# Optimization experiments

Measured on AMD Instinct MI355X. Metric: run time of the kernel, lower is better.

The kernel has to match this reference:

```python
import jax, jax.numpy as jnp
import numpy as np

NUM_QUBITS = 12
ENC_COPIES = 1
ANSATZ_COPIES = 2
BATCH = 1024
NUM_THETAS = NUM_QUBITS * (ANSATZ_COPIES + 1) * 2  # 72

_H = jnp.asarray(np.array([[1.0, 1.0], [1.0, -1.0]], np.complex64) / np.sqrt(2.0))


def _apply_1q(state, U, q):
    # state: [B, 2, 2, ..., 2] (n qubit axes); apply 2x2 unitary U on qubit q
    s = jnp.moveaxis(state, 1 + q, -1)
    s = jnp.einsum('...j,ij->...i', s, U)
    return jnp.moveaxis(s, -1, 1 + q)


def _apply_zpow(state, t, q):
    # cirq Z**t = diag(1, e^{i*pi*t}); t is scalar or per-batch [B]
    n = state.ndim - 1
    phase = jnp.exp(1j * jnp.pi * t).astype(jnp.complex64)
    factor = jnp.stack([jnp.ones_like(phase), phase], axis=-1)
    if factor.ndim == 2:  # batched exponent -> broadcast over other qubit axes
        factor = factor.reshape((factor.shape[0],) + (1,) * (n - 1) + (2,))
    s = jnp.moveaxis(state, 1 + q, -1)
    return jnp.moveaxis(s * factor, -1, 1 + q)


def _ypow_unitary(t):
    # cirq Y**t up to global phase e^{i*pi*t/2} (irrelevant for Z expectations)
    a = 0.5 * jnp.pi * t
    c, s = jnp.cos(a), jnp.sin(a)
    return jnp.stack([jnp.stack([c, -s]), jnp.stack([s, c])]).astype(jnp.complex64)


def _apply_cnot(state, c, t):
    s = jnp.moveaxis(state, (1 + c, 1 + t), (-2, -1))
    s = jnp.stack([s[..., 0, :], s[..., 1, ::-1]], axis=-2)
    return jnp.moveaxis(s, (-2, -1), (1 + c, 1 + t))


def _encoding_block(state, x):
    # FirstOrderPauliZEncoding: per copy, per qubit: H then Z**x_q
    for _ in range(ENC_COPIES):
        for q in range(NUM_QUBITS):
            state = _apply_1q(state, _H, q)
            state = _apply_zpow(state, x[:, q], q)
    return state


def _ansatz_block(state, th, with_cnot):
    # EfficientSU2 layer: Y**th[q,0], Z**th[q,1] per qubit, then CNOT chain
    for q in range(NUM_QUBITS):
        state = _apply_1q(state, _ypow_unitary(th[q, 0]), q)
        state = _apply_zpow(state, th[q, 1], q)
    if with_cnot:
        for q in range(NUM_QUBITS - 1):
            state = _apply_cnot(state, q, q + 1)
    return state


_enc = jax.checkpoint(_encoding_block)
_ans_cnot = jax.checkpoint(lambda st, th: _ansatz_block(st, th, True))
_ans_last = jax.checkpoint(lambda st, th: _ansatz_block(st, th, False))


def _circuit(inputs, thetas):
    b = inputs.shape[0]
    state = jnp.zeros((b, 2 ** NUM_QUBITS), jnp.complex64).at[:, 0].set(1.0)
    state = state.reshape((b,) + (2,) * NUM_QUBITS)
    state = _enc(state, inputs)
    th = thetas.reshape(ANSATZ_COPIES + 1, NUM_QUBITS, 2)
    for l in range(ANSATZ_COPIES + 1):
        state = (_ans_cnot if l < ANSATZ_COPIES else _ans_last)(state, th[l])
    # readouts: <Z_q> for each qubit
    probs = state.real ** 2 + state.imag ** 2
    exps = []
    for q in range(NUM_QUBITS):
        axes = tuple(a for a in range(1, NUM_QUBITS + 1) if a != 1 + q)
        p = probs.sum(axis=axes)  # [B, 2]
        exps.append(p[:, 0] - p[:, 1])
    return jnp.stack(exps, axis=-1)  # [B, NUM_QUBITS]


def setup_inputs() -> dict:
    key = jax.random.key(0)
    k1, k2 = jax.random.split(key)
    inputs = jax.random.uniform(k1, (BATCH, NUM_QUBITS), jnp.float32)
    thetas = jax.random.uniform(k2, (NUM_THETAS,), jnp.float32, minval=-1.0, maxval=1.0)
    return {"inputs": inputs, "thetas": thetas}


def reference(inputs, thetas):
    return _circuit(inputs, thetas)
```

## Files before the change

kernel.cpp:

```cpp
#include <hip/hip_runtime.h>


#define PI_F 3.14159265358979323846f
#define NR 32
#define PAD 66

__device__ __forceinline__ float2 cmul(float2 a, float2 b) {
    return make_float2(a.x*b.x - a.y*b.y, a.x*b.y + a.y*b.x);
}
__device__ __forceinline__ float2 cmulc(float2 a, float2 b) {
    return make_float2(a.x*b.x + a.y*b.y, a.y*b.x - a.x*b.y);
}

template<int RB>
__device__ __forceinline__ void ypow_reg(float2 (&a)[NR], float c, float s) {
    #pragma unroll
    for (int r0 = 0; r0 < NR; ++r0) {
        if ((r0 >> RB) & 1) continue;
        const int r1 = r0 | (1 << RB);
        float2 a0 = a[r0], a1 = a[r1];
        a[r0] = make_float2(c*a0.x - s*a1.x, c*a0.y - s*a1.y);
        a[r1] = make_float2(s*a0.x + c*a1.x, s*a0.y + c*a1.y);
    }
}

__device__ __forceinline__ void exchange_AB(float2 (&a)[NR], float2* buf,
                                            int w, int lane, float c6, float s6) {
    float2* wb = buf + w * (NR * PAD);
    __syncthreads();
    #pragma unroll
    for (int r = 0; r < NR; ++r)
        wb[r * PAD + (lane & 31) * 2 + (lane >> 5)] = a[r];
    __syncthreads();
    const int g = lane >> 1;
    const float k0 = (lane & 1) ? s6 : c6;
    const float k1 = (lane & 1) ? c6 : -s6;
    #pragma unroll
    for (int r = 0; r < NR; ++r) {
        float2 p0 = wb[g * PAD + r * 2];
        float2 p1 = wb[g * PAD + r * 2 + 1];
        a[r] = make_float2(k0*p0.x + k1*p1.x, k0*p0.y + k1*p1.y);
    }
}

__device__ __forceinline__ void exchange_BA(float2 (&a)[NR], float2* buf,
                                            int w, int lane, float c0, float s0) {
    __syncthreads();
    const int p6w = lane ^ (w << 5);
    #pragma unroll
    for (int r = 0; r < NR; ++r)
        buf[p6w * PAD + r * 2 + w] = a[r];
    __syncthreads();
    const float k0 = w ? s0 : c0;
    const float k1 = w ? c0 : -s0;
    #pragma unroll
    for (int rp = 0; rp < NR; ++rp) {
        const int ylow = (rp << 6) | lane;
        const int t = ylow ^ (ylow >> 1);
        const int base = (t >> 5) * PAD + (t & 31) * 2;
        float2 p0 = buf[base];
        float2 p1 = buf[base + 1];
        a[rp] = make_float2(k0*p0.x + k1*p1.x, k0*p0.y + k1*p1.y);
    }
}

__device__ __forceinline__ void ypow_block_regA(float2 (&a)[NR], const float* __restrict__ th) {
    { float s,c; __sincosf(0.5f*PI_F*th[2],  &s,&c); ypow_reg<4>(a,c,s); }
    { float s,c; __sincosf(0.5f*PI_F*th[4],  &s,&c); ypow_reg<3>(a,c,s); }
    { float s,c; __sincosf(0.5f*PI_F*th[6],  &s,&c); ypow_reg<2>(a,c,s); }
    { float s,c; __sincosf(0.5f*PI_F*th[8],  &s,&c); ypow_reg<1>(a,c,s); }
    { float s,c; __sincosf(0.5f*PI_F*th[10], &s,&c); ypow_reg<0>(a,c,s); }
}
__device__ __forceinline__ void ypow_block_regB(float2 (&a)[NR], const float* __restrict__ th) {
    { float s,c; __sincosf(0.5f*PI_F*th[14], &s,&c); ypow_reg<4>(a,c,s); }
    { float s,c; __sincosf(0.5f*PI_F*th[16], &s,&c); ypow_reg<3>(a,c,s); }
    { float s,c; __sincosf(0.5f*PI_F*th[18], &s,&c); ypow_reg<2>(a,c,s); }
    { float s,c; __sincosf(0.5f*PI_F*th[20], &s,&c); ypow_reg<1>(a,c,s); }
    { float s,c; __sincosf(0.5f*PI_F*th[22], &s,&c); ypow_reg<0>(a,c,s); }
}

__device__ __forceinline__ void fused_z_B(float2 (&a)[NR], int w, int lane,
                                          const float* __restrict__ th) {
    float alpha = w ? th[1] : 0.0f;
    #pragma unroll
    for (int k = 0; k < 6; ++k)
        alpha += ((lane >> k) & 1) ? th[2*(6-k)+1] : 0.0f;
    float2 zb; __sincosf(PI_F * alpha, &zb.y, &zb.x);
    float2 zq[5];
    #pragma unroll
    for (int j = 0; j < 5; ++j)
        __sincosf(PI_F * th[2*(11-j)+1], &zq[j].y, &zq[j].x);
    float2 cur = zb;
    a[0] = cmul(a[0], cur);
    #pragma unroll
    for (int k = 1; k < NR; ++k) {
        const int bit = __builtin_ctz(k);
        const int g = k ^ (k >> 1);
        cur = ((g >> bit) & 1) ? cmul(cur, zq[bit]) : cmulc(cur, zq[bit]);
        a[g] = cmul(a[g], cur);
    }
}

__global__ __launch_bounds__(128) void vqc_kernel(
    const float* __restrict__ inputs,
    const float* __restrict__ thetas,
    float* __restrict__ out)
{
    __shared__ __align__(16) float2 buf[64 * PAD];
    __shared__ float redBuf[24];

    const int b = blockIdx.x;
    const int tid = threadIdx.x;
    const int w = tid >> 6;
    const int lane = tid & 63;
    const float* x = inputs + b * 12;

    float2 a[NR];

    float phb = 0.0f;
    #pragma unroll
    for (int k = 0; k < 6; ++k)
        phb += ((lane >> k) & 1) ? x[11 - k] : 0.0f;
    float2 cisb; __sincosf(PI_F * phb, &cisb.y, &cisb.x);
    float2 E;    __sincosf(PI_F * x[0], &E.y, &E.x);
    float s0, c0; __sincosf(0.5f * PI_F * thetas[0], &s0, &c0);
    float2 Fw = w ? make_float2(s0 + c0 * E.x,  c0 * E.y)
                  : make_float2(c0 - s0 * E.x, -s0 * E.y);
    float2 g0 = cmul(Fw, cisb);
    g0.x *= 0.015625f; g0.y *= 0.015625f;
    float2 zr[5];
    #pragma unroll
    for (int j = 0; j < 5; ++j)
        __sincosf(PI_F * x[5 - j], &zr[j].y, &zr[j].x);
    {
        float2 cur = g0;
        a[0] = cur;
        #pragma unroll
        for (int k = 1; k < NR; ++k) {
            const int bit = __builtin_ctz(k);
            const int g = k ^ (k >> 1);
            cur = ((g >> bit) & 1) ? cmul(cur, zr[bit]) : cmulc(cur, zr[bit]);
            a[g] = cur;
        }
    }

    const float* th0 = thetas;
    const float* th1 = thetas + 24;
    const float* th2 = thetas + 48;

    ypow_block_regA(a, th0);
    { float s,c; __sincosf(0.5f*PI_F*th0[12], &s,&c); exchange_AB(a, buf, w, lane, c, s); }
    ypow_block_regB(a, th0);
    fused_z_B(a, w, lane, th0);
    { float s,c; __sincosf(0.5f*PI_F*th1[0],  &s,&c); exchange_BA(a, buf, w, lane, c, s); }

    ypow_block_regA(a, th1);
    { float s,c; __sincosf(0.5f*PI_F*th1[12], &s,&c); exchange_AB(a, buf, w, lane, c, s); }
    ypow_block_regB(a, th1);
    fused_z_B(a, w, lane, th1);
    { float s,c; __sincosf(0.5f*PI_F*th2[0],  &s,&c); exchange_BA(a, buf, w, lane, c, s); }

    ypow_block_regA(a, th2);
    { float s,c; __sincosf(0.5f*PI_F*th2[12], &s,&c); exchange_AB(a, buf, w, lane, c, s); }
    ypow_block_regB(a, th2);

    float totalP = 0.0f;
    float D[5] = {0, 0, 0, 0, 0};
    #pragma unroll
    for (int r = 0; r < NR; ++r) {
        const float p = a[r].x * a[r].x + a[r].y * a[r].y;
        totalP += p;
        #pragma unroll
        for (int j = 0; j < 5; ++j)
            D[j] += ((r >> j) & 1) ? -p : p;
    }
    #pragma unroll
    for (int q = 0; q < 12; ++q) {
        float v;
        if (q == 0)       v = w ? -totalP : totalP;
        else if (q <= 6)  v = ((lane >> (6 - q)) & 1) ? -totalP : totalP;
        else              v = D[11 - q];
        #pragma unroll
        for (int off = 32; off >= 1; off >>= 1)
            v += __shfl_xor(v, off, 64);
        if (lane == 0) redBuf[w * 12 + q] = v;
    }
    __syncthreads();
    if (tid < 12) out[b * 12 + tid] = redBuf[tid] + redBuf[12 + tid];
}

extern "C" void kernel_launch(void* const* d_in, const int* in_sizes, int n_in,
                              void* d_out, int out_size, void* d_ws, size_t ws_size,
                              hipStream_t stream) {
    const float* inputs = (const float*)d_in[0];
    const float* thetas = (const float*)d_in[1];
    float* out = (float*)d_out;
    vqc_kernel<<<dim3(1024), dim3(128), 0, stream>>>(inputs, thetas, out);
}
```

Before: 77.16 us.

## Process two batch elements per block with interleaved register state

Each 128-thread block now simulates two circuits at once, holding two 32-entry register state arrays and interleaving their gate updates. Shared-memory exchanges and barriers are amortised over both elements, and the Y rotation sincos values are computed once per layer and shared. The three layers move into a non-unrolled loop, and the grid is halved. In exchange, register pressure roughly doubles, fewer blocks are resident, and the intra-wave LDS exchange for the second element relies on wavefront ordering with no barrier between the two uses of the buffer.

```diff
diff --git a/kernel.cpp b/kernel.cpp
--- a/kernel.cpp
+++ b/kernel.cpp
@@ -24,14 +24,11 @@
     }
 }
 
-__device__ __forceinline__ void exchange_AB(float2 (&a)[NR], float2* buf,
-                                            int w, int lane, float c6, float s6) {
-    float2* wb = buf + w * (NR * PAD);
-    __syncthreads();
+__device__ __forceinline__ void exchange_AB_nb(float2 (&a)[NR], float2* wb,
+                                               int lane, float c6, float s6) {
     #pragma unroll
     for (int r = 0; r < NR; ++r)
         wb[r * PAD + (lane & 31) * 2 + (lane >> 5)] = a[r];
-    __syncthreads();
     const int g = lane >> 1;
     const float k0 = (lane & 1) ? s6 : c6;
     const float k1 = (lane & 1) ? c6 : -s6;
@@ -64,23 +61,8 @@
     }
 }
 
-__device__ __forceinline__ void ypow_block_regA(float2 (&a)[NR], const float* __restrict__ th) {
-    { float s,c; __sincosf(0.5f*PI_F*th[2],  &s,&c); ypow_reg<4>(a,c,s); }
-    { float s,c; __sincosf(0.5f*PI_F*th[4],  &s,&c); ypow_reg<3>(a,c,s); }
-    { float s,c; __sincosf(0.5f*PI_F*th[6],  &s,&c); ypow_reg<2>(a,c,s); }
-    { float s,c; __sincosf(0.5f*PI_F*th[8],  &s,&c); ypow_reg<1>(a,c,s); }
-    { float s,c; __sincosf(0.5f*PI_F*th[10], &s,&c); ypow_reg<0>(a,c,s); }
-}
-__device__ __forceinline__ void ypow_block_regB(float2 (&a)[NR], const float* __restrict__ th) {
-    { float s,c; __sincosf(0.5f*PI_F*th[14], &s,&c); ypow_reg<4>(a,c,s); }
-    { float s,c; __sincosf(0.5f*PI_F*th[16], &s,&c); ypow_reg<3>(a,c,s); }
-    { float s,c; __sincosf(0.5f*PI_F*th[18], &s,&c); ypow_reg<2>(a,c,s); }
-    { float s,c; __sincosf(0.5f*PI_F*th[20], &s,&c); ypow_reg<1>(a,c,s); }
-    { float s,c; __sincosf(0.5f*PI_F*th[22], &s,&c); ypow_reg<0>(a,c,s); }
-}
-
-__device__ __forceinline__ void fused_z_B(float2 (&a)[NR], int w, int lane,
-                                          const float* __restrict__ th) {
+__device__ __forceinline__ void fused_z_B2(float2 (&a0)[NR], float2 (&a1)[NR],
+                                           int w, int lane, const float* __restrict__ th) {
     float alpha = w ? th[1] : 0.0f;
     #pragma unroll
     for (int k = 0; k < 6; ++k)
@@ -91,39 +73,27 @@
     for (int j = 0; j < 5; ++j)
         __sincosf(PI_F * th[2*(11-j)+1], &zq[j].y, &zq[j].x);
     float2 cur = zb;
-    a[0] = cmul(a[0], cur);
+    a0[0] = cmul(a0[0], cur);
+    a1[0] = cmul(a1[0], cur);
     #pragma unroll
     for (int k = 1; k < NR; ++k) {
         const int bit = __builtin_ctz(k);
         const int g = k ^ (k >> 1);
         cur = ((g >> bit) & 1) ? cmul(cur, zq[bit]) : cmulc(cur, zq[bit]);
-        a[g] = cmul(a[g], cur);
-    }
-}
-
-__global__ __launch_bounds__(128) void vqc_kernel(
-    const float* __restrict__ inputs,
-    const float* __restrict__ thetas,
-    float* __restrict__ out)
-{
-    __shared__ __align__(16) float2 buf[64 * PAD];
-    __shared__ float redBuf[24];
-
-    const int b = blockIdx.x;
-    const int tid = threadIdx.x;
-    const int w = tid >> 6;
-    const int lane = tid & 63;
-    const float* x = inputs + b * 12;
-
-    float2 a[NR];
-
+        a0[g] = cmul(a0[g], cur);
+        a1[g] = cmul(a1[g], cur);
+    }
+}
+
+__device__ __forceinline__ void encode_init(float2 (&a)[NR], int w, int lane,
+                                            const float* __restrict__ x,
+                                            float c0, float s0) {
     float phb = 0.0f;
     #pragma unroll
     for (int k = 0; k < 6; ++k)
         phb += ((lane >> k) & 1) ? x[11 - k] : 0.0f;
     float2 cisb; __sincosf(PI_F * phb, &cisb.y, &cisb.x);
     float2 E;    __sincosf(PI_F * x[0], &E.y, &E.x);
-    float s0, c0; __sincosf(0.5f * PI_F * thetas[0], &s0, &c0);
     float2 Fw = w ? make_float2(s0 + c0 * E.x,  c0 * E.y)
                   : make_float2(c0 - s0 * E.x, -s0 * E.y);
     float2 g0 = cmul(Fw, cisb);
@@ -132,38 +102,19 @@
     #pragma unroll
     for (int j = 0; j < 5; ++j)
         __sincosf(PI_F * x[5 - j], &zr[j].y, &zr[j].x);
-    {
-        float2 cur = g0;
-        a[0] = cur;
-        #pragma unroll
-        for (int k = 1; k < NR; ++k) {
-            const int bit = __builtin_ctz(k);
-            const int g = k ^ (k >> 1);
-            cur = ((g >> bit) & 1) ? cmul(cur, zr[bit]) : cmulc(cur, zr[bit]);
-            a[g] = cur;
-        }
-    }
-
-    const float* th0 = thetas;
-    const float* th1 = thetas + 24;
-    const float* th2 = thetas + 48;
-
-    ypow_block_regA(a, th0);
-    { float s,c; __sincosf(0.5f*PI_F*th0[12], &s,&c); exchange_AB(a, buf, w, lane, c, s); }
-    ypow_block_regB(a, th0);
-    fused_z_B(a, w, lane, th0);
-    { float s,c; __sincosf(0.5f*PI_F*th1[0],  &s,&c); exchange_BA(a, buf, w, lane, c, s); }
-
-    ypow_block_regA(a, th1);
-    { float s,c; __sincosf(0.5f*PI_F*th1[12], &s,&c); exchange_AB(a, buf, w, lane, c, s); }
-    ypow_block_regB(a, th1);
-    fused_z_B(a, w, lane, th1);
-    { float s,c; __sincosf(0.5f*PI_F*th2[0],  &s,&c); exchange_BA(a, buf, w, lane, c, s); }
-
-    ypow_block_regA(a, th2);
-    { float s,c; __sincosf(0.5f*PI_F*th2[12], &s,&c); exchange_AB(a, buf, w, lane, c, s); }
-    ypow_block_regB(a, th2);
-
+    float2 cur = g0;
+    a[0] = cur;
+    #pragma unroll
+    for (int k = 1; k < NR; ++k) {
+        const int bit = __builtin_ctz(k);
+        const int g = k ^ (k >> 1);
+        cur = ((g >> bit) & 1) ? cmul(cur, zr[bit]) : cmulc(cur, zr[bit]);
+        a[g] = cur;
+    }
+}
+
+__device__ __forceinline__ void readout(const float2 (&a)[NR], int w, int lane,
+                                        float* __restrict__ red) {
     float totalP = 0.0f;
     float D[5] = {0, 0, 0, 0, 0};
     #pragma unroll
@@ -183,10 +134,70 @@
         #pragma unroll
         for (int off = 32; off >= 1; off >>= 1)
             v += __shfl_xor(v, off, 64);
-        if (lane == 0) redBuf[w * 12 + q] = v;
-    }
+        if (lane == 0) red[w * 12 + q] = v;
+    }
+}
+
+__global__ __launch_bounds__(128) void vqc_kernel(
+    const float* __restrict__ inputs,
+    const float* __restrict__ thetas,
+    float* __restrict__ out)
+{
+    __shared__ __align__(16) float2 buf[64 * PAD];
+    __shared__ float redBuf[2][24];
+
+    const int b0 = blockIdx.x * 2;
+    const int tid = threadIdx.x;
+    const int w = tid >> 6;
+    const int lane = tid & 63;
+    const float* x0 = inputs + b0 * 12;
+    const float* x1 = x0 + 12;
+
+    float2 a0[NR], a1[NR];
+
+    float s00, c00; __sincosf(0.5f * PI_F * thetas[0], &s00, &c00);
+    encode_init(a0, w, lane, x0, c00, s00);
+    encode_init(a1, w, lane, x1, c00, s00);
+
+    #pragma unroll 1
+    for (int l = 0; l < 3; ++l) {
+        const float* th = thetas + l * 24;
+        float yc[12], ys[12];
+        #pragma unroll
+        for (int q = 0; q < 12; ++q)
+            __sincosf(0.5f * PI_F * th[2 * q], &ys[q], &yc[q]);
+
+        ypow_reg<4>(a0, yc[1], ys[1]); ypow_reg<4>(a1, yc[1], ys[1]);
+        ypow_reg<3>(a0, yc[2], ys[2]); ypow_reg<3>(a1, yc[2], ys[2]);
+        ypow_reg<2>(a0, yc[3], ys[3]); ypow_reg<2>(a1, yc[3], ys[3]);
+        ypow_reg<1>(a0, yc[4], ys[4]); ypow_reg<1>(a1, yc[4], ys[4]);
+        ypow_reg<0>(a0, yc[5], ys[5]); ypow_reg<0>(a1, yc[5], ys[5]);
+
+        __syncthreads();
+        exchange_AB_nb(a0, buf + w * (NR * PAD), lane, yc[6], ys[6]);
+        exchange_AB_nb(a1, buf + w * (NR * PAD), lane, yc[6], ys[6]);
+
+        ypow_reg<4>(a0, yc[7],  ys[7]);  ypow_reg<4>(a1, yc[7],  ys[7]);
+        ypow_reg<3>(a0, yc[8],  ys[8]);  ypow_reg<3>(a1, yc[8],  ys[8]);
+        ypow_reg<2>(a0, yc[9],  ys[9]);  ypow_reg<2>(a1, yc[9],  ys[9]);
+        ypow_reg<1>(a0, yc[10], ys[10]); ypow_reg<1>(a1, yc[10], ys[10]);
+        ypow_reg<0>(a0, yc[11], ys[11]); ypow_reg<0>(a1, yc[11], ys[11]);
+
+        if (l < 2) {
+            fused_z_B2(a0, a1, w, lane, th);
+            float sn, cn; __sincosf(0.5f * PI_F * th[24], &sn, &cn);
+            exchange_BA(a0, buf, w, lane, cn, sn);
+            exchange_BA(a1, buf, w, lane, cn, sn);
+        }
+    }
+
+    readout(a0, w, lane, redBuf[0]);
+    readout(a1, w, lane, redBuf[1]);
     __syncthreads();
-    if (tid < 12) out[b * 12 + tid] = redBuf[tid] + redBuf[12 + tid];
+    if (tid < 24) {
+        const int e = tid / 12, q = tid - e * 12;
+        out[(b0 + e) * 12 + q] = redBuf[e][q] + redBuf[e][12 + q];
+    }
 }
 
 extern "C" void kernel_launch(void* const* d_in, const int* in_sizes, int n_in,
@@ -195,5 +206,5 @@
     const float* inputs = (const float*)d_in[0];
     const float* thetas = (const float*)d_in[1];
     float* out = (float*)d_out;
-    vqc_kernel<<<dim3(1024), dim3(128), 0, stream>>>(inputs, thetas, out);
-}
+    vqc_kernel<<<dim3(512), dim3(128), 0, stream>>>(inputs, thetas, out);
+}
```

After: 81.20 us. +5.2%, slower.

## Split state over four waves and fold first ansatz layer into analytic product-state init

Applied to the files above, without the earlier changes.

Each block now runs 256 threads holding 16 amplitudes each instead of 128 threads holding 32, so two qubits are distributed across waves rather than one. The encoding plus the first ansatz layer, which has no CNOT chain, is computed analytically as a product state, removing one full exchange round and its rotations. The shared-memory exchanges now apply two Y rotations per pass with new padded layouts. This is meant to cut register pressure and raise occupancy, at the cost of more threads per block and more complex indexing.

```diff
diff --git a/kernel.cpp b/kernel.cpp
--- a/kernel.cpp
+++ b/kernel.cpp
@@ -2,14 +2,12 @@
 
 
 #define PI_F 3.14159265358979323846f
-#define NR 32
-#define PAD 66
+#define NR 16
+#define ROWP_BA 129
+#define ROWP_AB 66
 
 __device__ __forceinline__ float2 cmul(float2 a, float2 b) {
     return make_float2(a.x*b.x - a.y*b.y, a.x*b.y + a.y*b.x);
-}
-__device__ __forceinline__ float2 cmulc(float2 a, float2 b) {
-    return make_float2(a.x*b.x + a.y*b.y, a.y*b.x - a.x*b.y);
 }
 
 template<int RB>
@@ -24,169 +22,206 @@
     }
 }
 
-__device__ __forceinline__ void exchange_AB(float2 (&a)[NR], float2* buf,
-                                            int w, int lane, float c6, float s6) {
-    float2* wb = buf + w * (NR * PAD);
+__device__ __forceinline__ void exchange_BA(float2 (&a)[NR], float2* buf,
+                                            int w, int lane,
+                                            float c0, float s0, float c1, float s1,
+                                            bool first) {
+    if (!first) __syncthreads();
+    const int wbase = (lane & 31) * ROWP_BA + (lane >> 5) * 4 + w;
+    #pragma unroll
+    for (int r = 0; r < NR; ++r)
+        buf[wbase + r * 8] = a[r];
     __syncthreads();
-    #pragma unroll
-    for (int r = 0; r < NR; ++r)
-        wb[r * PAD + (lane & 31) * 2 + (lane >> 5)] = a[r];
-    __syncthreads();
-    const int g = lane >> 1;
-    const float k0 = (lane & 1) ? s6 : c6;
-    const float k1 = (lane & 1) ? c6 : -s6;
-    #pragma unroll
-    for (int r = 0; r < NR; ++r) {
-        float2 p0 = wb[g * PAD + r * 2];
-        float2 p1 = wb[g * PAD + r * 2 + 1];
-        a[r] = make_float2(k0*p0.x + k1*p1.x, k0*p0.y + k1*p1.y);
-    }
-}
-
-__device__ __forceinline__ void exchange_BA(float2 (&a)[NR], float2* buf,
-                                            int w, int lane, float c0, float s0) {
-    __syncthreads();
-    const int p6w = lane ^ (w << 5);
-    #pragma unroll
-    for (int r = 0; r < NR; ++r)
-        buf[p6w * PAD + r * 2 + w] = a[r];
-    __syncthreads();
-    const float k0 = w ? s0 : c0;
-    const float k1 = w ? c0 : -s0;
+    const float y0a = (w & 2) ? s0 : c0;
+    const float y0b = (w & 2) ? c0 : -s0;
+    const float y1a = (w & 1) ? s1 : c1;
+    const float y1b = (w & 1) ? c1 : -s1;
+    const float K00 = y0a*y1a, K01 = y0a*y1b, K10 = y0b*y1a, K11 = y0b*y1b;
     #pragma unroll
     for (int rp = 0; rp < NR; ++rp) {
         const int ylow = (rp << 6) | lane;
         const int t = ylow ^ (ylow >> 1);
-        const int base = (t >> 5) * PAD + (t & 31) * 2;
-        float2 p0 = buf[base];
-        float2 p1 = buf[base + 1];
-        a[rp] = make_float2(k0*p0.x + k1*p1.x, k0*p0.y + k1*p1.y);
-    }
-}
-
-__device__ __forceinline__ void ypow_block_regA(float2 (&a)[NR], const float* __restrict__ th) {
-    { float s,c; __sincosf(0.5f*PI_F*th[2],  &s,&c); ypow_reg<4>(a,c,s); }
-    { float s,c; __sincosf(0.5f*PI_F*th[4],  &s,&c); ypow_reg<3>(a,c,s); }
-    { float s,c; __sincosf(0.5f*PI_F*th[6],  &s,&c); ypow_reg<2>(a,c,s); }
-    { float s,c; __sincosf(0.5f*PI_F*th[8],  &s,&c); ypow_reg<1>(a,c,s); }
-    { float s,c; __sincosf(0.5f*PI_F*th[10], &s,&c); ypow_reg<0>(a,c,s); }
-}
-__device__ __forceinline__ void ypow_block_regB(float2 (&a)[NR], const float* __restrict__ th) {
-    { float s,c; __sincosf(0.5f*PI_F*th[14], &s,&c); ypow_reg<4>(a,c,s); }
-    { float s,c; __sincosf(0.5f*PI_F*th[16], &s,&c); ypow_reg<3>(a,c,s); }
-    { float s,c; __sincosf(0.5f*PI_F*th[18], &s,&c); ypow_reg<2>(a,c,s); }
-    { float s,c; __sincosf(0.5f*PI_F*th[20], &s,&c); ypow_reg<1>(a,c,s); }
-    { float s,c; __sincosf(0.5f*PI_F*th[22], &s,&c); ypow_reg<0>(a,c,s); }
+        const int base = ((t >> 4) & 31) * ROWP_BA + (t & 15) * 8;
+        const int x9 = (rp >> 3) & 1;
+        float2 i00 = buf[base + x9 * 4 + 0];
+        float2 i01 = buf[base + (x9 ^ 1) * 4 + 1];
+        float2 i10 = buf[base + x9 * 4 + 3];
+        float2 i11 = buf[base + (x9 ^ 1) * 4 + 2];
+        a[rp] = make_float2(K00*i00.x + K01*i01.x + K10*i10.x + K11*i11.x,
+                            K00*i00.y + K01*i01.y + K10*i10.y + K11*i11.y);
+    }
+}
+
+__device__ __forceinline__ void exchange_AB(float2 (&a)[NR], float2* wbuf,
+                                            int lane,
+                                            float c6, float s6, float c7, float s7) {
+    __syncthreads();
+    const int wslot = (lane & 15) * 4 + (lane >> 4);
+    #pragma unroll
+    for (int r = 0; r < NR; ++r)
+        wbuf[r * ROWP_AB + wslot] = a[r];
+    const int j = lane & 3;
+    const float e0 = (j & 2) ? s6 : c6;
+    const float e1 = (j & 2) ? c6 : -s6;
+    const float f0 = (j & 1) ? s7 : c7;
+    const float f1 = (j & 1) ? c7 : -s7;
+    const float C0 = e0*f0, C1 = e0*f1, C2 = e1*f0, C3 = e1*f1;
+    const int rbase = (lane >> 2) * ROWP_AB;
+    #pragma unroll
+    for (int rp = 0; rp < NR; ++rp) {
+        float2 p0 = wbuf[rbase + rp * 4 + 0];
+        float2 p1 = wbuf[rbase + rp * 4 + 1];
+        float2 p2 = wbuf[rbase + rp * 4 + 2];
+        float2 p3 = wbuf[rbase + rp * 4 + 3];
+        a[rp] = make_float2(C0*p0.x + C1*p1.x + C2*p2.x + C3*p3.x,
+                            C0*p0.y + C1*p1.y + C2*p2.y + C3*p3.y);
+    }
 }
 
 __device__ __forceinline__ void fused_z_B(float2 (&a)[NR], int w, int lane,
                                           const float* __restrict__ th) {
-    float alpha = w ? th[1] : 0.0f;
+    float alpha = 0.0f;
+    if (w & 2) alpha += th[1];
+    if (w & 1) alpha += th[3];
     #pragma unroll
     for (int k = 0; k < 6; ++k)
-        alpha += ((lane >> k) & 1) ? th[2*(6-k)+1] : 0.0f;
-    float2 zb; __sincosf(PI_F * alpha, &zb.y, &zb.x);
-    float2 zq[5];
-    #pragma unroll
-    for (int j = 0; j < 5; ++j)
-        __sincosf(PI_F * th[2*(11-j)+1], &zq[j].y, &zq[j].x);
-    float2 cur = zb;
-    a[0] = cmul(a[0], cur);
-    #pragma unroll
-    for (int k = 1; k < NR; ++k) {
-        const int bit = __builtin_ctz(k);
-        const int g = k ^ (k >> 1);
-        cur = ((g >> bit) & 1) ? cmul(cur, zq[bit]) : cmulc(cur, zq[bit]);
-        a[g] = cmul(a[g], cur);
-    }
-}
-
-__global__ __launch_bounds__(128) void vqc_kernel(
+        alpha += ((lane >> k) & 1) ? th[2*(7-k)+1] : 0.0f;
+    float2 cA; __sincosf(PI_F * alpha, &cA.y, &cA.x);
+    float2 z8, z9, z10, z11;
+    __sincosf(PI_F * th[17], &z8.y,  &z8.x);
+    __sincosf(PI_F * th[19], &z9.y,  &z9.x);
+    __sincosf(PI_F * th[21], &z10.y, &z10.x);
+    __sincosf(PI_F * th[23], &z11.y, &z11.x);
+    float2 hi[4], lo[4];
+    hi[0] = cA;                    hi[1] = cmul(cA, z9);
+    hi[2] = cmul(cA, z8);          hi[3] = cmul(hi[2], z9);
+    lo[0] = make_float2(1.f, 0.f); lo[1] = z11;
+    lo[2] = z10;                   lo[3] = cmul(z10, z11);
+    #pragma unroll
+    for (int r = 0; r < NR; ++r)
+        a[r] = cmul(cmul(a[r], hi[r >> 2]), lo[r & 3]);
+}
+
+__device__ __forceinline__ void encode_init(float2 (&a)[NR], int w, int lane,
+                                            const float* __restrict__ x,
+                                            const float* __restrict__ th0) {
+    float2 F = make_float2(0.015625f, 0.0f);
+    #pragma unroll
+    for (int q = 0; q < 8; ++q) {
+        float2 ex; __sincosf(PI_F * x[q], &ex.y, &ex.x);
+        float sy, cy; __sincosf(0.5f * PI_F * th0[2*q], &sy, &cy);
+        float2 cz; __sincosf(PI_F * th0[2*q+1], &cz.y, &cz.x);
+        float2 u0 = make_float2(cy - sy*ex.x, -sy*ex.y);
+        float2 u1 = cmul(cz, make_float2(sy + cy*ex.x, cy*ex.y));
+        int bit;
+        if (q == 0)      bit = (w >> 1) & 1;
+        else if (q == 1) bit = w & 1;
+        else             bit = (lane >> (7 - q)) & 1;
+        F = cmul(F, bit ? u1 : u0);
+    }
+    float2 v0[4], v1[4];
+    #pragma unroll
+    for (int q = 8; q < 12; ++q) {
+        float2 ex; __sincosf(PI_F * x[q], &ex.y, &ex.x);
+        float sy, cy; __sincosf(0.5f * PI_F * th0[2*q], &sy, &cy);
+        float2 cz; __sincosf(PI_F * th0[2*q+1], &cz.y, &cz.x);
+        v0[q-8] = make_float2(cy - sy*ex.x, -sy*ex.y);
+        v1[q-8] = cmul(cz, make_float2(sy + cy*ex.x, cy*ex.y));
+    }
+    float2 hi[4], lo[4];
+    hi[0] = cmul(v0[0], v0[1]); hi[1] = cmul(v0[0], v1[1]);
+    hi[2] = cmul(v1[0], v0[1]); hi[3] = cmul(v1[0], v1[1]);
+    lo[0] = cmul(v0[2], v0[3]); lo[1] = cmul(v0[2], v1[3]);
+    lo[2] = cmul(v1[2], v0[3]); lo[3] = cmul(v1[2], v1[3]);
+    #pragma unroll
+    for (int t = 0; t < 4; ++t) hi[t] = cmul(F, hi[t]);
+    #pragma unroll
+    for (int r = 0; r < NR; ++r)
+        a[r] = cmul(hi[r >> 2], lo[r & 3]);
+}
+
+__global__ __launch_bounds__(256, 4) void vqc_kernel(
     const float* __restrict__ inputs,
     const float* __restrict__ thetas,
     float* __restrict__ out)
 {
-    __shared__ __align__(16) float2 buf[64 * PAD];
-    __shared__ float redBuf[24];
+    __shared__ __align__(16) float2 buf[4 * NR * ROWP_AB];
+    __shared__ float redBuf[4][12];
 
     const int b = blockIdx.x;
     const int tid = threadIdx.x;
     const int w = tid >> 6;
     const int lane = tid & 63;
     const float* x = inputs + b * 12;
-
-    float2 a[NR];
-
-    float phb = 0.0f;
-    #pragma unroll
-    for (int k = 0; k < 6; ++k)
-        phb += ((lane >> k) & 1) ? x[11 - k] : 0.0f;
-    float2 cisb; __sincosf(PI_F * phb, &cisb.y, &cisb.x);
-    float2 E;    __sincosf(PI_F * x[0], &E.y, &E.x);
-    float s0, c0; __sincosf(0.5f * PI_F * thetas[0], &s0, &c0);
-    float2 Fw = w ? make_float2(s0 + c0 * E.x,  c0 * E.y)
-                  : make_float2(c0 - s0 * E.x, -s0 * E.y);
-    float2 g0 = cmul(Fw, cisb);
-    g0.x *= 0.015625f; g0.y *= 0.015625f;
-    float2 zr[5];
-    #pragma unroll
-    for (int j = 0; j < 5; ++j)
-        __sincosf(PI_F * x[5 - j], &zr[j].y, &zr[j].x);
-    {
-        float2 cur = g0;
-        a[0] = cur;
-        #pragma unroll
-        for (int k = 1; k < NR; ++k) {
-            const int bit = __builtin_ctz(k);
-            const int g = k ^ (k >> 1);
-            cur = ((g >> bit) & 1) ? cmul(cur, zr[bit]) : cmulc(cur, zr[bit]);
-            a[g] = cur;
-        }
-    }
-
-    const float* th0 = thetas;
     const float* th1 = thetas + 24;
     const float* th2 = thetas + 48;
 
-    ypow_block_regA(a, th0);
-    { float s,c; __sincosf(0.5f*PI_F*th0[12], &s,&c); exchange_AB(a, buf, w, lane, c, s); }
-    ypow_block_regB(a, th0);
-    fused_z_B(a, w, lane, th0);
-    { float s,c; __sincosf(0.5f*PI_F*th1[0],  &s,&c); exchange_BA(a, buf, w, lane, c, s); }
-
-    ypow_block_regA(a, th1);
-    { float s,c; __sincosf(0.5f*PI_F*th1[12], &s,&c); exchange_AB(a, buf, w, lane, c, s); }
-    ypow_block_regB(a, th1);
+    float2 a[NR];
+    encode_init(a, w, lane, x, thetas);
+
+    { float s0,c0,s1,c1;
+      __sincosf(0.5f*PI_F*th1[0], &s0, &c0);
+      __sincosf(0.5f*PI_F*th1[2], &s1, &c1);
+      exchange_BA(a, buf, w, lane, c0, s0, c1, s1, true); }
+
+    { float s,c; __sincosf(0.5f*PI_F*th1[4],  &s,&c); ypow_reg<3>(a,c,s); }
+    { float s,c; __sincosf(0.5f*PI_F*th1[6],  &s,&c); ypow_reg<2>(a,c,s); }
+    { float s,c; __sincosf(0.5f*PI_F*th1[8],  &s,&c); ypow_reg<1>(a,c,s); }
+    { float s,c; __sincosf(0.5f*PI_F*th1[10], &s,&c); ypow_reg<0>(a,c,s); }
+    { float s6,c6,s7,c7;
+      __sincosf(0.5f*PI_F*th1[12], &s6,&c6);
+      __sincosf(0.5f*PI_F*th1[14], &s7,&c7);
+      exchange_AB(a, buf + w * (NR * ROWP_AB), lane, c6, s6, c7, s7); }
+    { float s,c; __sincosf(0.5f*PI_F*th1[16], &s,&c); ypow_reg<3>(a,c,s); }
+    { float s,c; __sincosf(0.5f*PI_F*th1[18], &s,&c); ypow_reg<2>(a,c,s); }
+    { float s,c; __sincosf(0.5f*PI_F*th1[20], &s,&c); ypow_reg<1>(a,c,s); }
+    { float s,c; __sincosf(0.5f*PI_F*th1[22], &s,&c); ypow_reg<0>(a,c,s); }
     fused_z_B(a, w, lane, th1);
-    { float s,c; __sincosf(0.5f*PI_F*th2[0],  &s,&c); exchange_BA(a, buf, w, lane, c, s); }
-
-    ypow_block_regA(a, th2);
-    { float s,c; __sincosf(0.5f*PI_F*th2[12], &s,&c); exchange_AB(a, buf, w, lane, c, s); }
-    ypow_block_regB(a, th2);
+
+    { float s0,c0,s1,c1;
+      __sincosf(0.5f*PI_F*th2[0], &s0, &c0);
+      __sincosf(0.5f*PI_F*th2[2], &s1, &c1);
+      exchange_BA(a, buf, w, lane, c0, s0, c1, s1, false); }
+
+    { float s,c; __sincosf(0.5f*PI_F*th2[4],  &s,&c); ypow_reg<3>(a,c,s); }
+    { float s,c; __sincosf(0.5f*PI_F*th2[6],  &s,&c); ypow_reg<2>(a,c,s); }
+    { float s,c; __sincosf(0.5f*PI_F*th2[8],  &s,&c); ypow_reg<1>(a,c,s); }
+    { float s,c; __sincosf(0.5f*PI_F*th2[10], &s,&c); ypow_reg<0>(a,c,s); }
+    { float s6,c6,s7,c7;
+      __sincosf(0.5f*PI_F*th2[12], &s6,&c6);
+      __sincosf(0.5f*PI_F*th2[14], &s7,&c7);
+      exchange_AB(a, buf + w * (NR * ROWP_AB), lane, c6, s6, c7, s7); }
+    { float s,c; __sincosf(0.5f*PI_F*th2[16], &s,&c); ypow_reg<3>(a,c,s); }
+    { float s,c; __sincosf(0.5f*PI_F*th2[18], &s,&c); ypow_reg<2>(a,c,s); }
+    { float s,c; __sincosf(0.5f*PI_F*th2[20], &s,&c); ypow_reg<1>(a,c,s); }
+    { float s,c; __sincosf(0.5f*PI_F*th2[22], &s,&c); ypow_reg<0>(a,c,s); }
 
     float totalP = 0.0f;
-    float D[5] = {0, 0, 0, 0, 0};
+    float D[4] = {0, 0, 0, 0};
     #pragma unroll
     for (int r = 0; r < NR; ++r) {
         const float p = a[r].x * a[r].x + a[r].y * a[r].y;
         totalP += p;
         #pragma unroll
-        for (int j = 0; j < 5; ++j)
+        for (int j = 0; j < 4; ++j)
             D[j] += ((r >> j) & 1) ? -p : p;
     }
     #pragma unroll
     for (int q = 0; q < 12; ++q) {
         float v;
-        if (q == 0)       v = w ? -totalP : totalP;
-        else if (q <= 6)  v = ((lane >> (6 - q)) & 1) ? -totalP : totalP;
-        else              v = D[11 - q];
+        if (q == 0)      v = (w & 2) ? -totalP : totalP;
+        else if (q == 1) v = (w & 1) ? -totalP : totalP;
+        else if (q <= 7) v = ((lane >> (7 - q)) & 1) ? -totalP : totalP;
+        else             v = D[11 - q];
         #pragma unroll
         for (int off = 32; off >= 1; off >>= 1)
             v += __shfl_xor(v, off, 64);
-        if (lane == 0) redBuf[w * 12 + q] = v;
+        if (lane == 0) redBuf[w][q] = v;
     }
     __syncthreads();
-    if (tid < 12) out[b * 12 + tid] = redBuf[tid] + redBuf[12 + tid];
+    if (tid < 12)
+        out[b * 12 + tid] = redBuf[0][tid] + redBuf[1][tid]
+                          + redBuf[2][tid] + redBuf[3][tid];
 }
 
 extern "C" void kernel_launch(void* const* d_in, const int* in_sizes, int n_in,
@@ -195,5 +230,5 @@
     const float* inputs = (const float*)d_in[0];
     const float* thetas = (const float*)d_in[1];
     float* out = (float*)d_out;
-    vqc_kernel<<<dim3(1024), dim3(128), 0, stream>>>(inputs, thetas, out);
-}
+    vqc_kernel<<<dim3(1024), dim3(256), 0, stream>>>(inputs, thetas, out);
+}
```

Result: slower. 101.8 us (+31.9%).
